# Kernel tuning notes

Measured on AMD Instinct MI355X. Metric: run time of the kernel, lower is better.

## Reference

```python
import jax, jax.numpy as jnp
import numpy as np
import math

B, S, D, H, FF, NB = 32, 512, 512, 8, 2048, 2
DK = D // H  # 64
NEG = -1e30  # stands in for torch's -1e32 (fp32-safe)


def _make_pe():
    # CosinePositionalEmbedding: deterministic sin/cos part (the 0.1*randn is fully overwritten)
    pos = np.arange(S, dtype=np.float32)[:, None]
    div = np.exp(np.arange(0, D, 2, dtype=np.float32) * -(math.log(10000.0) / D))
    pe = np.zeros((S, D), np.float32)
    pe[:, 0::2] = np.sin(pos * div)
    pe[:, 1::2] = np.cos(pos * div)
    return jnp.asarray(pe)[None]  # [1, S, D]


def setup_inputs() -> dict:
    key = jax.random.key(0)
    ks = jax.random.split(key, 10)
    def w(k, shape):
        return jax.random.normal(k, shape, jnp.float32) * 0.02
    return {
        "q_embed_data": jax.random.normal(ks[0], (B, S, D), jnp.float32),
        "qa_embed_data": jax.random.normal(ks[1], (B, S, D), jnp.float32),
        "forget_rate": jax.random.uniform(ks[2], (B, 1, S, 1), jnp.float32),
        "pe": _make_pe(),
        "Wk": w(ks[3], (NB, D, D)), "bk": jnp.zeros((NB, D), jnp.float32),
        "Wv": w(ks[4], (NB, D, D)), "bv": jnp.zeros((NB, D), jnp.float32),
        "Wo": w(ks[5], (NB, D, D)), "bo": jnp.zeros((NB, D), jnp.float32),
        "g1": jnp.ones((NB, D), jnp.float32), "be1": jnp.zeros((NB, D), jnp.float32),
        "W1": w(ks[6], (NB, D, FF)), "bf1": jnp.zeros((NB, FF), jnp.float32),
        "W2": w(ks[7], (NB, FF, D)), "bf2": jnp.zeros((NB, D), jnp.float32),
        "g2": jnp.ones((NB, D), jnp.float32), "be2": jnp.zeros((NB, D), jnp.float32),
    }


def _ln(x, g, b):
    m = jnp.mean(x, axis=-1, keepdims=True)
    v = jnp.var(x, axis=-1, keepdims=True)
    return (x - m) * jax.lax.rsqrt(v + 1e-5) * g + b


def reference(q_embed_data, qa_embed_data, forget_rate, pe, Wk, bk, Wv, bv, Wo, bo,
              g1, be1, W1, bf1, W2, bf2, g2, be2):
    x = q_embed_data + pe[:, :S]   # query stream
    y = qa_embed_data + pe[:, :S]  # value stream (constant across blocks)
    # mask==0 path: src_mask True where triu(k=0)==0, i.e. strictly-past positions j < i
    allowed = jnp.tril(jnp.ones((S, S), bool), k=-1)
    scale = 1.0 / math.sqrt(DK)
    for i in range(NB):
        # kq_same=True: q and k both use k_linear; query=key=x so q == k
        q = (x @ Wk[i] + bk[i]).reshape(B, S, H, DK).transpose(0, 2, 1, 3)  # [B,H,S,dk]
        k = q
        v = (y @ Wv[i] + bv[i]).reshape(B, S, H, DK).transpose(0, 2, 1, 3)
        scores = jnp.einsum('bhqd,bhkd->bhqk', q, k) * scale      # [B,H,S,S]
        scores = scores * forget_rate                              # broadcast [B,1,S,1]
        scores = jnp.where(allowed, scores, NEG)                   # masked_fill(mask==0, -1e32)
        attn = jax.nn.softmax(scores, axis=-1)
        attn = attn.at[:, :, 0, :].set(0.0)                        # zero_pad first query row
        out = jnp.einsum('bhqk,bhkd->bhqd', attn, v)
        out = out.transpose(0, 2, 1, 3).reshape(B, S, D) @ Wo[i] + bo[i]
        x = _ln(x + out, g1[i], be1[i])
        ffn = jax.nn.relu(x @ W1[i] + bf1[i]) @ W2[i] + bf2[i]
        x = _ln(x + ffn, g2[i], be2[i])
    return x
```

## Files before the change

### kernel.cpp

```cpp
#include <hip/hip_runtime.h>

#define B_ 32
#define S_ 512
#define D_ 512
#define H_ 8
#define DK_ 64
#define FF_ 2048

typedef float f32x4 __attribute__((ext_vector_type(4)));
typedef __bf16 bf16x8 __attribute__((ext_vector_type(8)));
typedef __bf16 bf16x4 __attribute__((ext_vector_type(4)));

__device__ __forceinline__ void gld_lds16(const void* gptr, void* lptr) {
    auto g = (__attribute__((address_space(1))) void*)(unsigned long long)gptr;
    auto l = (__attribute__((address_space(3))) void*)(unsigned)(unsigned long long)lptr;
    __builtin_amdgcn_global_load_lds(g, l, 16, 0, 0);
}

__global__ __launch_bounds__(256) void prep_kernel(
    const float* __restrict__ q, const float* __restrict__ qa,
    const float* __restrict__ pe, __bf16* __restrict__ xbf,
    __bf16* __restrict__ ybf)
{
    const int n4 = B_ * S_ * D_ / 4;
    for (int i = blockIdx.x * blockDim.x + threadIdx.x; i < n4;
         i += gridDim.x * blockDim.x) {
        float4 pv = ((const float4*)pe)[i & (S_ * D_ / 4 - 1)];
        float4 qv = ((const float4*)q)[i];
        float4 av = ((const float4*)qa)[i];
        bf16x4 xb = {(__bf16)(qv.x + pv.x), (__bf16)(qv.y + pv.y),
                     (__bf16)(qv.z + pv.z), (__bf16)(qv.w + pv.w)};
        ((bf16x4*)xbf)[i] = xb;
        bf16x4 yb = {(__bf16)(av.x + pv.x), (__bf16)(av.y + pv.y),
                     (__bf16)(av.z + pv.z), (__bf16)(av.w + pv.w)};
        ((bf16x4*)ybf)[i] = yb;
    }
}

__device__ __forceinline__ void ttile(
    const float* __restrict__ in, __bf16* __restrict__ out,
    int R, int C, int bx, int by, int t)
{
    __shared__ float tile[32][33];
    const int tc = bx * 32, tr = by * 32;
    const int lx = t & 31, ly = t >> 5;
    #pragma unroll
    for (int yy = ly; yy < 32; yy += 8)
        tile[yy][lx] = in[(long)(tr + yy) * C + tc + lx];
    __syncthreads();
    #pragma unroll
    for (int yy = ly; yy < 32; yy += 8)
        out[(long)(tc + yy) * R + tr + lx] = (__bf16)tile[lx][yy];
}

__global__ __launch_bounds__(256) void transpose_all(
    const float* __restrict__ Wk, const float* __restrict__ Wv,
    const float* __restrict__ Wo, const float* __restrict__ W1,
    const float* __restrict__ W2, __bf16* __restrict__ ok,
    __bf16* __restrict__ ov, __bf16* __restrict__ oo,
    __bf16* __restrict__ o1, __bf16* __restrict__ o2)
{
    const int id = blockIdx.x, t = threadIdx.x;
    if (id < 1536) {
        const int z = id >> 8, r = id & 255;
        const int sel = z >> 1, i = z & 1;
        const float* src = sel == 0 ? Wk : (sel == 1 ? Wv : Wo);
        __bf16* dst = sel == 0 ? ok : (sel == 1 ? ov : oo);
        ttile(src + (long)i * 262144, dst + (long)i * 262144, 512, 512,
              r & 15, r >> 4, t);
    } else if (id < 3584) {
        int r = id - 1536; const int i = r >> 10; r &= 1023;
        ttile(W1 + (long)i * 1048576, o1 + (long)i * 1048576, 512, 2048,
              r & 63, r >> 6, t);
    } else {
        int r = id - 3584; const int i = r >> 10; r &= 1023;
        ttile(W2 + (long)i * 1048576, o2 + (long)i * 1048576, 2048, 512,
              r & 15, r >> 4, t);
    }
}

template <int RELU, int MODE>
__global__ __launch_bounds__(256) void gemm_kernel(
    const __bf16* __restrict__ A, const __bf16* __restrict__ Bt,
    const float* __restrict__ bias, const __bf16* __restrict__ res,
    __bf16* __restrict__ out, int M, int N, int K)
{
    __shared__ __bf16 As[2][128 * 64];
    __shared__ __bf16 Bs[2][128 * 64];
    const int t = threadIdx.x;
    const int lane = t & 63;
    const int wv = t >> 6, wr = wv >> 1, wc = wv & 1;
    const int lr = lane & 15, lk = lane >> 4;

    const int nwg = gridDim.x * gridDim.y;
    const int lin = blockIdx.y * gridDim.x + blockIdx.x;
    const int swz = (lin & 7) * (nwg >> 3) + (lin >> 3);
    const int m0 = (swz / gridDim.x) * 128, n0 = (swz % gridDim.x) * 128;

    const int srow = t >> 3;
    const int sslot = (t & 7) ^ (srow & 7);
    const __bf16* gA = A + (long)(m0 + srow) * K + sslot * 8;
    const __bf16* gB = Bt + (long)(n0 + srow) * K + sslot * 8;
    const long rstep = (long)32 * K;

    auto STAGE = [&](int bsel, int k0) {
        char* ldsA = (char*)As[bsel] + t * 16;
        char* ldsB = (char*)Bs[bsel] + t * 16;
        #pragma unroll
        for (int u = 0; u < 4; ++u) {
            gld_lds16(gA + u * rstep + k0, ldsA + u * 4096);
            gld_lds16(gB + u * rstep + k0, ldsB + u * 4096);
        }
    };

    f32x4 acc[4][4] = {};
    auto COMPUTE = [&](int bsel) {
        #pragma unroll
        for (int kk = 0; kk < 2; ++kk) {
            bf16x8 af[4], bfr[4];
            #pragma unroll
            for (int i = 0; i < 4; ++i) {
                const int rr = wr * 64 + i * 16 + lr;
                af[i] = *(const bf16x8*)((const char*)As[bsel] +
                        (rr << 7) + (((kk * 4 + lk) ^ (rr & 7)) << 4));
            }
            #pragma unroll
            for (int j = 0; j < 4; ++j) {
                const int rr = wc * 64 + j * 16 + lr;
                bfr[j] = *(const bf16x8*)((const char*)Bs[bsel] +
                         (rr << 7) + (((kk * 4 + lk) ^ (rr & 7)) << 4));
            }
            #pragma unroll
            for (int i = 0; i < 4; ++i)
                #pragma unroll
                for (int j = 0; j < 4; ++j)
                    acc[i][j] = __builtin_amdgcn_mfma_f32_16x16x32_bf16(
                        af[i], bfr[j], acc[i][j], 0, 0, 0);
        }
    };

    const int NT = K >> 6;
    STAGE(0, 0);
    STAGE(1, 64);
    for (int kt = 0; kt < NT - 1; ++kt) {
        asm volatile("s_waitcnt vmcnt(8)" ::: "memory");
        __builtin_amdgcn_s_barrier();
        COMPUTE(kt & 1);
        __builtin_amdgcn_s_barrier();
        if (kt + 2 < NT) STAGE(kt & 1, (kt + 2) << 6);
    }
    asm volatile("s_waitcnt vmcnt(0)" ::: "memory");
    __builtin_amdgcn_s_barrier();
    COMPUTE((NT - 1) & 1);

    #pragma unroll
    for (int i = 0; i < 4; ++i) {
        #pragma unroll
        for (int j = 0; j < 4; ++j) {
            const int n = n0 + wc * 64 + j * 16 + lr;
            const float bv = bias[n];
            #pragma unroll
            for (int r = 0; r < 4; ++r) {
                const int m = m0 + wr * 64 + i * 16 + lk * 4 + r;
                const long off = (long)m * N + n;
                float v = acc[i][j][r] + bv;
                if (MODE == 1) v += (float)res[off];
                if (RELU) v = v > 0.f ? v : 0.f;
                out[off] = (__bf16)v;
            }
        }
    }
}

template <int RELU, int MODE>
__global__ __launch_bounds__(512, 2) void gemm8_kernel(
    const __bf16* __restrict__ A, const __bf16* __restrict__ Bt,
    const float* __restrict__ bias, const __bf16* __restrict__ res,
    __bf16* __restrict__ out, int M, int N, int K)
{
    __shared__ __bf16 lds[65536];
    const int t = threadIdx.x;
    const int lane = t & 63, wv = t >> 6;
    const int wr = wv >> 2, wc = wv & 3;
    const int lr = lane & 15, lk = lane >> 4;

    const int nwg = gridDim.x * gridDim.y;
    const int lin = blockIdx.y * gridDim.x + blockIdx.x;
    const int swz = (lin & 7) * (nwg >> 3) + (lin >> 3);
    const int m0 = (swz / gridDim.x) * 256, n0 = (swz % gridDim.x) * 256;

    const int srcrow = lane >> 2;
    const int srccol = ((lane & 3) ^ ((lane >> 4) & 3)) * 8;
    auto STG = [&](int isB, int kt2, int kk2, int pb) {
        const __bf16* src = isB ? Bt : A;
        const int base = isB ? n0 : m0;
        #pragma unroll
        for (int u = 0; u < 2; ++u) {
            const int sr = u * 8 + wv;
            const long g = (long)(base + sr * 16 + srcrow) * K + kt2 * 64 + kk2 * 32 + srccol;
            char* d = (char*)lds + pb * 65536 + isB * 32768 + ((sr * 2 + kk2) << 10) + lane * 16;
            gld_lds16(src + g, d);
        }
    };

    f32x4 acc[8][4] = {};
    bf16x8 af[4], bfr[4];
    auto RDA = [&](int p, int kk, int mh) {
        #pragma unroll
        for (int i = 0; i < 4; ++i) {
            const int sr = wr * 8 + mh * 4 + i;
            af[i] = *(const bf16x8*)((const char*)lds + p * 65536 +
                    ((sr * 2 + kk) << 10) + lr * 64 + ((lk ^ ((lr >> 2) & 3)) << 4));
        }
    };
    auto RDB = [&](int p, int kk) {
        #pragma unroll
        for (int j = 0; j < 4; ++j) {
            const int sr = wc * 4 + j;
            bfr[j] = *(const bf16x8*)((const char*)lds + p * 65536 + 32768 +
                     ((sr * 2 + kk) << 10) + lr * 64 + ((lk ^ ((lr >> 2) & 3)) << 4));
        }
    };
    auto MM = [&](int mh) {
        __builtin_amdgcn_s_setprio(1);
        #pragma unroll
        for (int i = 0; i < 4; ++i)
            #pragma unroll
            for (int j = 0; j < 4; ++j)
                acc[mh * 4 + i][j] = __builtin_amdgcn_mfma_f32_16x16x32_bf16(
                    af[i], bfr[j], acc[mh * 4 + i][j], 0, 0, 0);
        __builtin_amdgcn_s_setprio(0);
    };

    const int NT = K >> 6;
    STG(0, 0, 0, 0); STG(1, 0, 0, 0); STG(0, 0, 1, 0); STG(1, 0, 1, 0);
    STG(0, 1, 0, 1); STG(1, 1, 0, 1);

    for (int kt = 0; kt < NT - 1; ++kt) {
        const int p = kt & 1;
        asm volatile("s_waitcnt vmcnt(8)" ::: "memory");
        __builtin_amdgcn_s_barrier();
        RDA(p, 0, 0); RDB(p, 0); STG(0, kt + 1, 1, p ^ 1);
        MM(0);
        __builtin_amdgcn_s_barrier();
        RDA(p, 0, 1); STG(1, kt + 1, 1, p ^ 1);
        MM(1);
        asm volatile("s_waitcnt vmcnt(8)" ::: "memory");
        __builtin_amdgcn_s_barrier();
        RDA(p, 1, 0); RDB(p, 1); if (kt + 2 < NT) STG(0, kt + 2, 0, p);
        MM(0);
        __builtin_amdgcn_s_barrier();
        RDA(p, 1, 1); if (kt + 2 < NT) STG(1, kt + 2, 0, p);
        MM(1);
    }
    {
        const int p = (NT - 1) & 1;
        asm volatile("s_waitcnt vmcnt(4)" ::: "memory");
        __builtin_amdgcn_s_barrier();
        RDA(p, 0, 0); RDB(p, 0); MM(0);
        __builtin_amdgcn_s_barrier();
        RDA(p, 0, 1); MM(1);
        asm volatile("s_waitcnt vmcnt(0)" ::: "memory");
        __builtin_amdgcn_s_barrier();
        RDA(p, 1, 0); RDB(p, 1); MM(0);
        __builtin_amdgcn_s_barrier();
        RDA(p, 1, 1); MM(1);
    }

    #pragma unroll
    for (int i = 0; i < 8; ++i) {
        #pragma unroll
        for (int j = 0; j < 4; ++j) {
            const int n = n0 + wc * 64 + j * 16 + lr;
            const float bv = bias[n];
            #pragma unroll
            for (int r = 0; r < 4; ++r) {
                const int m = m0 + wr * 128 + i * 16 + lk * 4 + r;
                const long off = (long)m * N + n;
                float v = acc[i][j][r] + bv;
                if (MODE == 1) v += (float)res[off];
                if (RELU) v = v > 0.f ? v : 0.f;
                out[off] = (__bf16)v;
            }
        }
    }
}

__global__ __launch_bounds__(256) void gemm_kv(
    const __bf16* __restrict__ xbf, const __bf16* __restrict__ ybf,
    const __bf16* __restrict__ wkt, const __bf16* __restrict__ wvt,
    const float* __restrict__ bk, const float* __restrict__ bv,
    __bf16* __restrict__ kout, __bf16* __restrict__ vtout)
{
    constexpr int N = 512, K = 512;
    __shared__ __bf16 As[2][128 * 64];
    __shared__ __bf16 Bs[2][128 * 64];
    const int t = threadIdx.x;
    const int lane = t & 63;
    const int wv = t >> 6, wr = wv >> 1, wc = wv & 1;
    const int lr = lane & 15, lk = lane >> 4;
    const int zv = blockIdx.z;

    const __bf16* A  = zv ? ybf : xbf;
    const __bf16* Bt = zv ? wvt : wkt;
    const float* bias = zv ? bv : bk;
    __bf16* out = zv ? vtout : kout;

    const int nwg = gridDim.x * gridDim.y;
    const int lin = blockIdx.y * gridDim.x + blockIdx.x;
    const int swz = (lin & 7) * (nwg >> 3) + (lin >> 3);
    const int m0 = (swz / gridDim.x) * 128, n0 = (swz % gridDim.x) * 128;

    const int srow = t >> 3;
    const int sslot = (t & 7) ^ (srow & 7);
    const __bf16* gA = A + (long)(m0 + srow) * K + sslot * 8;
    const __bf16* gB = Bt + (long)(n0 + srow) * K + sslot * 8;
    const long rstep = (long)32 * K;

    auto STAGE = [&](int bsel, int k0) {
        char* ldsA = (char*)As[bsel] + t * 16;
        char* ldsB = (char*)Bs[bsel] + t * 16;
        #pragma unroll
        for (int u = 0; u < 4; ++u) {
            gld_lds16(gA + u * rstep + k0, ldsA + u * 4096);
            gld_lds16(gB + u * rstep + k0, ldsB + u * 4096);
        }
    };

    f32x4 acc[4][4] = {};
    auto COMPUTE = [&](int bsel) {
        #pragma unroll
        for (int kk = 0; kk < 2; ++kk) {
            bf16x8 af[4], bfr[4];
            #pragma unroll
            for (int i = 0; i < 4; ++i) {
                const int rr = wr * 64 + i * 16 + lr;
                af[i] = *(const bf16x8*)((const char*)As[bsel] +
                        (rr << 7) + (((kk * 4 + lk) ^ (rr & 7)) << 4));
            }
            #pragma unroll
            for (int j = 0; j < 4; ++j) {
                const int rr = wc * 64 + j * 16 + lr;
                bfr[j] = *(const bf16x8*)((const char*)Bs[bsel] +
                         (rr << 7) + (((kk * 4 + lk) ^ (rr & 7)) << 4));
            }
            #pragma unroll
            for (int i = 0; i < 4; ++i)
                #pragma unroll
                for (int j = 0; j < 4; ++j)
                    acc[i][j] = __builtin_amdgcn_mfma_f32_16x16x32_bf16(
                        af[i], bfr[j], acc[i][j], 0, 0, 0);
        }
    };

    const int NT = K >> 6;
    STAGE(0, 0);
    STAGE(1, 64);
    for (int kt = 0; kt < NT - 1; ++kt) {
        asm volatile("s_waitcnt vmcnt(8)" ::: "memory");
        __builtin_amdgcn_s_barrier();
        COMPUTE(kt & 1);
        __builtin_amdgcn_s_barrier();
        if (kt + 2 < NT) STAGE(kt & 1, (kt + 2) << 6);
    }
    asm volatile("s_waitcnt vmcnt(0)" ::: "memory");
    __builtin_amdgcn_s_barrier();
    COMPUTE((NT - 1) & 1);

    #pragma unroll
    for (int i = 0; i < 4; ++i) {
        #pragma unroll
        for (int j = 0; j < 4; ++j) {
            const int n = n0 + wc * 64 + j * 16 + lr;
            const float bvl = bias[n];
            if (zv) {
                const int mb = m0 + wr * 64 + i * 16 + lk * 4;
                const int b = mb >> 9, s = mb & 511;
                bf16x4 ov = {(__bf16)(acc[i][j][0] + bvl),
                             (__bf16)(acc[i][j][1] + bvl),
                             (__bf16)(acc[i][j][2] + bvl),
                             (__bf16)(acc[i][j][3] + bvl)};
                *(bf16x4*)(out + (((long)(b * 8 + (n >> 6)) * 64 + (n & 63)) << 9) + s) = ov;
            } else {
                #pragma unroll
                for (int r = 0; r < 4; ++r) {
                    const int m = m0 + wr * 64 + i * 16 + lk * 4 + r;
                    out[(long)m * N + n] = (__bf16)(acc[i][j][r] + bvl);
                }
            }
        }
    }
}

__global__ __launch_bounds__(256) void attn_kernel(
    const __bf16* __restrict__ Q, const __bf16* __restrict__ Vt,
    const float* __restrict__ fr, __bf16* __restrict__ Out)
{
    __shared__ __bf16 Ks[2][64 * 64];
    __shared__ __bf16 Vs[2][64 * 64];
    __shared__ __bf16 Plds[4][16 * 64];
    const int t = threadIdx.x;
    const int lane = t & 63, wv = t >> 6;
    const int lr = lane & 15, lk = lane >> 4;
    const int qb = blockIdx.x, h = blockIdx.y, b = blockIdx.z;
    const int qT = qb * 64 + wv * 16;

    const __bf16* qp = Q + (long)(b * S_ + qT + lr) * D_ + h * DK_ + lk * 8;
    const bf16x8 qf0 = *(const bf16x8*)qp;
    const bf16x8 qf1 = *(const bf16x8*)(qp + 32);

    float frv[4], ls[4];
    #pragma unroll
    for (int r = 0; r < 4; ++r) {
        frv[r] = fr[b * S_ + qT + lk * 4 + r] * 0.125f;
        ls[r] = 0.f;
    }
    f32x4 o[4] = {};

    const int srow = t >> 3;
    const int sslot = (t & 7) ^ (srow & 7);
    const __bf16* kstage = Q + (long)(b * S_ + srow) * D_ + h * DK_ + sslot * 8;
    const __bf16* vstage = Vt + ((long)(b * H_ + h) * DK_ + srow) * S_ + sslot * 8;
    __bf16* pl = &Plds[wv][0];
    const int sw = (lr & 7);

    auto STAGE = [&](int bsel, int ks) {
        gld_lds16(kstage + (long)ks * D_, (char*)Ks[bsel] + t * 16);
        gld_lds16(kstage + (long)(ks + 32) * D_, (char*)Ks[bsel] + 4096 + t * 16);
        gld_lds16(vstage + ks, (char*)Vs[bsel] + t * 16);
        gld_lds16(vstage + ks + 32 * S_, (char*)Vs[bsel] + 4096 + t * 16);
    };

    auto COMPUTE = [&](int bsel, int ks) {
        f32x4 sc[4] = {};
        #pragma unroll
        for (int j = 0; j < 4; ++j) {
            const char* kb = (const char*)Ks[bsel] + ((j * 16 + lr) << 7);
            const bf16x8 kf0 = *(const bf16x8*)(kb + ((lk ^ sw) << 4));
            const bf16x8 kf1 = *(const bf16x8*)(kb + (((lk + 4) ^ sw) << 4));
            sc[j] = __builtin_amdgcn_mfma_f32_16x16x32_bf16(qf0, kf0, sc[j], 0, 0, 0);
            sc[j] = __builtin_amdgcn_mfma_f32_16x16x32_bf16(qf1, kf1, sc[j], 0, 0, 0);
        }
        #pragma unroll
        for (int j = 0; j < 4; ++j) {
            const int col = ks + j * 16 + lr;
            const int c8 = j * 2 + (lr >> 3), cb = lr & 7;
            #pragma unroll
            for (int r = 0; r < 4; ++r) {
                const int row = lk * 4 + r;
                const int sidx = row * 64 + ((c8 ^ (row & 7)) << 3) + cb;
                const float e = __expf(sc[j][r] * frv[r]);
                const float p = (col < qT + row) ? e : 0.f;
                ls[r] += p;
                pl[sidx] = (__bf16)p;
            }
        }
        bf16x8 pf[2];
        #pragma unroll
        for (int kk = 0; kk < 2; ++kk) {
            const int ridx = lr * 64 + (((kk * 4 + lk) ^ sw) << 3);
            pf[kk] = *(const bf16x8*)&pl[ridx];
        }
        #pragma unroll
        for (int dt = 0; dt < 4; ++dt) {
            const char* vb = (const char*)Vs[bsel] + ((dt * 16 + lr) << 7);
            #pragma unroll
            for (int kk = 0; kk < 2; ++kk) {
                const bf16x8 vf = *(const bf16x8*)(vb + (((kk * 4 + lk) ^ sw) << 4));
                o[dt] = __builtin_amdgcn_mfma_f32_16x16x32_bf16(pf[kk], vf, o[dt], 0, 0, 0);
            }
        }
    };

    const int nt = qb + 1;
    STAGE(0, 0);
    if (nt > 1) STAGE(1, 64);
    for (int tt = 0; tt < nt - 1; ++tt) {
        asm volatile("s_waitcnt vmcnt(4)" ::: "memory");
        __builtin_amdgcn_s_barrier();
        COMPUTE(tt & 1, tt * 64);
        __builtin_amdgcn_s_barrier();
        if (tt + 2 < nt) STAGE(tt & 1, (tt + 2) * 64);
    }
    asm volatile("s_waitcnt vmcnt(0)" ::: "memory");
    __builtin_amdgcn_s_barrier();
    COMPUTE((nt - 1) & 1, (nt - 1) * 64);

    #pragma unroll
    for (int r = 0; r < 4; ++r) {
        #pragma unroll
        for (int d = 1; d < 16; d <<= 1)
            ls[r] += __shfl_xor(ls[r], d);
        const float inv = ls[r] > 0.f ? 1.f / ls[r] : 0.f;
        #pragma unroll
        for (int dt = 0; dt < 4; ++dt)
            Out[(long)(b * S_ + qT + lk * 4 + r) * D_ + h * DK_ + dt * 16 + lr] =
                (__bf16)(o[dt][r] * inv);
    }
}

__global__ __launch_bounds__(256) void ln_kernel(
    const __bf16* __restrict__ pre, const float* __restrict__ g,
    const float* __restrict__ be, float* __restrict__ xout,
    __bf16* __restrict__ xbf, int wf32)
{
    const int lane = threadIdx.x & 63, wv = threadIdx.x >> 6;
    const long row = (long)blockIdx.x * 4 + wv;
    const bf16x8 v = *(const bf16x8*)(pre + row * D_ + lane * 8);
    float f[8];
    #pragma unroll
    for (int k = 0; k < 8; ++k) f[k] = (float)v[k];
    float s = 0.f, ss = 0.f;
    #pragma unroll
    for (int k = 0; k < 8; ++k) { s += f[k]; ss += f[k] * f[k]; }
    #pragma unroll
    for (int d = 1; d < 64; d <<= 1) {
        s  += __shfl_xor(s, d);
        ss += __shfl_xor(ss, d);
    }
    const float mean = s * (1.f / 512.f);
    const float rstd = rsqrtf(ss * (1.f / 512.f) - mean * mean + 1e-5f);
    const float4 ga = ((const float4*)(g + lane * 8))[0];
    const float4 gc = ((const float4*)(g + lane * 8))[1];
    const float4 ba = ((const float4*)(be + lane * 8))[0];
    const float4 bc = ((const float4*)(be + lane * 8))[1];
    float o[8];
    o[0] = (f[0] - mean) * rstd * ga.x + ba.x;
    o[1] = (f[1] - mean) * rstd * ga.y + ba.y;
    o[2] = (f[2] - mean) * rstd * ga.z + ba.z;
    o[3] = (f[3] - mean) * rstd * ga.w + ba.w;
    o[4] = (f[4] - mean) * rstd * gc.x + bc.x;
    o[5] = (f[5] - mean) * rstd * gc.y + bc.y;
    o[6] = (f[6] - mean) * rstd * gc.z + bc.z;
    o[7] = (f[7] - mean) * rstd * gc.w + bc.w;
    bf16x8 xb = {(__bf16)o[0], (__bf16)o[1], (__bf16)o[2], (__bf16)o[3],
                 (__bf16)o[4], (__bf16)o[5], (__bf16)o[6], (__bf16)o[7]};
    *(bf16x8*)(xbf + row * D_ + lane * 8) = xb;
    if (wf32) {
        float* xo = xout + row * D_ + lane * 8;
        ((float4*)xo)[0] = make_float4(o[0], o[1], o[2], o[3]);
        ((float4*)xo)[1] = make_float4(o[4], o[5], o[6], o[7]);
    }
}

extern "C" void kernel_launch(void* const* d_in, const int* in_sizes, int n_in,
                              void* d_out, int out_size, void* d_ws, size_t ws_size,
                              hipStream_t stream) {
    const float* q_embed = (const float*)d_in[0];
    const float* qa_embed = (const float*)d_in[1];
    const float* fr  = (const float*)d_in[2];
    const float* pe  = (const float*)d_in[3];
    const float* Wk  = (const float*)d_in[4];
    const float* bk  = (const float*)d_in[5];
    const float* Wv  = (const float*)d_in[6];
    const float* bv  = (const float*)d_in[7];
    const float* Wo  = (const float*)d_in[8];
    const float* bo  = (const float*)d_in[9];
    const float* g1  = (const float*)d_in[10];
    const float* be1 = (const float*)d_in[11];
    const float* W1  = (const float*)d_in[12];
    const float* bf1 = (const float*)d_in[13];
    const float* W2  = (const float*)d_in[14];
    const float* bf2 = (const float*)d_in[15];
    const float* g2  = (const float*)d_in[16];
    const float* be2 = (const float*)d_in[17];

    char* ws = (char*)d_ws;
    __bf16* xbf   = (__bf16*)(ws + 0);
    __bf16* ybf   = (__bf16*)(ws + 16777216);
    __bf16* pool  = (__bf16*)(ws + 33554432);
    __bf16* preln = (__bf16*)(ws + 100663296);
    __bf16* wts   = (__bf16*)(ws + 117440512);

    __bf16* kbuf  = pool;
    __bf16* vtbuf = pool + 8388608;
    __bf16* abuf  = pool + 2 * 8388608;
    __bf16* f1buf = pool;

    __bf16* wkt = wts;
    __bf16* wvt = wts + 524288;
    __bf16* wot = wts + 1048576;
    __bf16* w1t = wts + 1572864;
    __bf16* w2t = wts + 3670016;

    transpose_all<<<5632, 256, 0, stream>>>(Wk, Wv, Wo, W1, W2,
                                            wkt, wvt, wot, w1t, w2t);
    prep_kernel<<<2048, 256, 0, stream>>>(q_embed, qa_embed, pe, xbf, ybf);

    for (int i = 0; i < 2; ++i) {
        gemm_kv<<<dim3(4, 128, 2), 256, 0, stream>>>(
            xbf, ybf, wkt + i * 262144, wvt + i * 262144,
            bk + i * 512, bv + i * 512, kbuf, vtbuf);
        attn_kernel<<<dim3(8, 8, 32), 256, 0, stream>>>(kbuf, vtbuf, fr, abuf);
        gemm_kernel<0, 1><<<dim3(4, 128), 256, 0, stream>>>(
            abuf, wot + i * 262144, bo + i * 512, xbf, preln, 16384, 512, 512);
        ln_kernel<<<4096, 256, 0, stream>>>(preln, g1 + i * 512, be1 + i * 512,
                                            (float*)d_out, xbf, 0);
        gemm8_kernel<1, 0><<<dim3(8, 64), 512, 0, stream>>>(
            xbf, w1t + i * 1048576, bf1 + i * 2048, nullptr, f1buf, 16384, 2048, 512);
        gemm_kernel<0, 1><<<dim3(4, 128), 256, 0, stream>>>(
            f1buf, w2t + i * 1048576, bf2 + i * 512, xbf, preln, 16384, 512, 2048);
        ln_kernel<<<4096, 256, 0, stream>>>(preln, g2 + i * 512, be2 + i * 512,
                                            (float*)d_out, xbf, i == 1 ? 1 : 0);
    }
}
```

Before: 432.2 us.

## Merge prep into weight-transpose launch, stage V-transpose epilogue via LDS, fold GEMM tail

Folds the input embedding/PE-add conversion into the weight-transpose kernel so both run in one launch. The gemm8 main loop absorbs its peeled final iteration, and its wait counts change to vmcnt(4) once per iteration with vmcnt(0) on the last. The K/V GEMM's transposed V output is now staged through swizzled shared memory and written as 16-byte row segments instead of scattered 8-byte stores. These target launch overhead and uncoalesced transposed writes, at the cost of an extra LDS round trip and two block barriers in the epilogue.

```diff
diff --git a/kernel.cpp b/kernel.cpp
--- a/kernel.cpp
+++ b/kernel.cpp
@@ -15,26 +15,6 @@
     auto g = (__attribute__((address_space(1))) void*)(unsigned long long)gptr;
     auto l = (__attribute__((address_space(3))) void*)(unsigned)(unsigned long long)lptr;
     __builtin_amdgcn_global_load_lds(g, l, 16, 0, 0);
-}
-
-__global__ __launch_bounds__(256) void prep_kernel(
-    const float* __restrict__ q, const float* __restrict__ qa,
-    const float* __restrict__ pe, __bf16* __restrict__ xbf,
-    __bf16* __restrict__ ybf)
-{
-    const int n4 = B_ * S_ * D_ / 4;
-    for (int i = blockIdx.x * blockDim.x + threadIdx.x; i < n4;
-         i += gridDim.x * blockDim.x) {
-        float4 pv = ((const float4*)pe)[i & (S_ * D_ / 4 - 1)];
-        float4 qv = ((const float4*)q)[i];
-        float4 av = ((const float4*)qa)[i];
-        bf16x4 xb = {(__bf16)(qv.x + pv.x), (__bf16)(qv.y + pv.y),
-                     (__bf16)(qv.z + pv.z), (__bf16)(qv.w + pv.w)};
-        ((bf16x4*)xbf)[i] = xb;
-        bf16x4 yb = {(__bf16)(av.x + pv.x), (__bf16)(av.y + pv.y),
-                     (__bf16)(av.z + pv.z), (__bf16)(av.w + pv.w)};
-        ((bf16x4*)ybf)[i] = yb;
-    }
 }
 
 __device__ __forceinline__ void ttile(
@@ -53,12 +33,15 @@
         out[(long)(tc + yy) * R + tr + lx] = (__bf16)tile[lx][yy];
 }
 
-__global__ __launch_bounds__(256) void transpose_all(
+__global__ __launch_bounds__(256) void pre_all(
     const float* __restrict__ Wk, const float* __restrict__ Wv,
     const float* __restrict__ Wo, const float* __restrict__ W1,
-    const float* __restrict__ W2, __bf16* __restrict__ ok,
-    __bf16* __restrict__ ov, __bf16* __restrict__ oo,
-    __bf16* __restrict__ o1, __bf16* __restrict__ o2)
+    const float* __restrict__ W2, const float* __restrict__ q,
+    const float* __restrict__ qa, const float* __restrict__ pe,
+    __bf16* __restrict__ ok, __bf16* __restrict__ ov,
+    __bf16* __restrict__ oo, __bf16* __restrict__ o1,
+    __bf16* __restrict__ o2, __bf16* __restrict__ xbf,
+    __bf16* __restrict__ ybf)
 {
     const int id = blockIdx.x, t = threadIdx.x;
     if (id < 1536) {
@@ -72,10 +55,23 @@
         int r = id - 1536; const int i = r >> 10; r &= 1023;
         ttile(W1 + (long)i * 1048576, o1 + (long)i * 1048576, 512, 2048,
               r & 63, r >> 6, t);
-    } else {
+    } else if (id < 5632) {
         int r = id - 3584; const int i = r >> 10; r &= 1023;
         ttile(W2 + (long)i * 1048576, o2 + (long)i * 1048576, 2048, 512,
               r & 15, r >> 4, t);
+    } else {
+        const int n4 = B_ * S_ * D_ / 4;
+        for (int i = (id - 5632) * 256 + t; i < n4; i += 2048 * 256) {
+            float4 pv = ((const float4*)pe)[i & (S_ * D_ / 4 - 1)];
+            float4 qv = ((const float4*)q)[i];
+            float4 av = ((const float4*)qa)[i];
+            bf16x4 xb = {(__bf16)(qv.x + pv.x), (__bf16)(qv.y + pv.y),
+                         (__bf16)(qv.z + pv.z), (__bf16)(qv.w + pv.w)};
+            ((bf16x4*)xbf)[i] = xb;
+            bf16x4 yb = {(__bf16)(av.x + pv.x), (__bf16)(av.y + pv.y),
+                         (__bf16)(av.z + pv.z), (__bf16)(av.w + pv.w)};
+            ((bf16x4*)ybf)[i] = yb;
+        }
     }
 }
 
@@ -236,35 +232,22 @@
     STG(0, 0, 0, 0); STG(1, 0, 0, 0); STG(0, 0, 1, 0); STG(1, 0, 1, 0);
     STG(0, 1, 0, 1); STG(1, 1, 0, 1);
 
-    for (int kt = 0; kt < NT - 1; ++kt) {
+    for (int kt = 0; kt < NT; ++kt) {
         const int p = kt & 1;
-        asm volatile("s_waitcnt vmcnt(8)" ::: "memory");
-        __builtin_amdgcn_s_barrier();
-        RDA(p, 0, 0); RDB(p, 0); STG(0, kt + 1, 1, p ^ 1);
+        if (kt == NT - 1) asm volatile("s_waitcnt vmcnt(0)" ::: "memory");
+        else              asm volatile("s_waitcnt vmcnt(4)" ::: "memory");
+        __builtin_amdgcn_s_barrier();
+        RDA(p, 0, 0); RDB(p, 0); if (kt + 1 < NT) STG(0, kt + 1, 1, p ^ 1);
         MM(0);
         __builtin_amdgcn_s_barrier();
-        RDA(p, 0, 1); STG(1, kt + 1, 1, p ^ 1);
+        RDA(p, 0, 1); if (kt + 1 < NT) STG(1, kt + 1, 1, p ^ 1);
         MM(1);
-        asm volatile("s_waitcnt vmcnt(8)" ::: "memory");
         __builtin_amdgcn_s_barrier();
         RDA(p, 1, 0); RDB(p, 1); if (kt + 2 < NT) STG(0, kt + 2, 0, p);
         MM(0);
         __builtin_amdgcn_s_barrier();
         RDA(p, 1, 1); if (kt + 2 < NT) STG(1, kt + 2, 0, p);
         MM(1);
-    }
-    {
-        const int p = (NT - 1) & 1;
-        asm volatile("s_waitcnt vmcnt(4)" ::: "memory");
-        __builtin_amdgcn_s_barrier();
-        RDA(p, 0, 0); RDB(p, 0); MM(0);
-        __builtin_amdgcn_s_barrier();
-        RDA(p, 0, 1); MM(1);
-        asm volatile("s_waitcnt vmcnt(0)" ::: "memory");
-        __builtin_amdgcn_s_barrier();
-        RDA(p, 1, 0); RDB(p, 1); MM(0);
-        __builtin_amdgcn_s_barrier();
-        RDA(p, 1, 1); MM(1);
     }
 
     #pragma unroll
@@ -367,21 +350,48 @@
     __builtin_amdgcn_s_barrier();
     COMPUTE((NT - 1) & 1);
 
-    #pragma unroll
-    for (int i = 0; i < 4; ++i) {
-        #pragma unroll
-        for (int j = 0; j < 4; ++j) {
-            const int n = n0 + wc * 64 + j * 16 + lr;
-            const float bvl = bias[n];
-            if (zv) {
-                const int mb = m0 + wr * 64 + i * 16 + lk * 4;
-                const int b = mb >> 9, s = mb & 511;
-                bf16x4 ov = {(__bf16)(acc[i][j][0] + bvl),
-                             (__bf16)(acc[i][j][1] + bvl),
-                             (__bf16)(acc[i][j][2] + bvl),
-                             (__bf16)(acc[i][j][3] + bvl)};
-                *(bf16x4*)(out + (((long)(b * 8 + (n >> 6)) * 64 + (n & 63)) << 9) + s) = ov;
-            } else {
+    if (zv) {
+        __syncthreads();
+        __bf16* st = (__bf16*)As;
+        #pragma unroll
+        for (int i = 0; i < 4; ++i) {
+            #pragma unroll
+            for (int j = 0; j < 4; ++j) {
+                const int nl = wc * 64 + j * 16 + lr;
+                const float bvl = bias[n0 + nl];
+                #pragma unroll
+                for (int r = 0; r < 4; ++r) {
+                    const int ml = wr * 64 + i * 16 + lk * 4 + r;
+                    const int m16 = ml >> 3;
+                    st[nl * 128 + (((m16 ^ (nl & 15)) << 3) | (ml & 7))] =
+                        (__bf16)(acc[i][j][r] + bvl);
+                }
+            }
+        }
+        __syncthreads();
+        const int rowh = t >> 2, c4 = t & 3;
+        const int b = m0 >> 9;
+        #pragma unroll
+        for (int pass = 0; pass < 2; ++pass) {
+            const int row = pass * 64 + rowh;
+            const int n = n0 + row;
+            __bf16* dst = out + (((long)((b * 8 + (n >> 6)) * 64 + (n & 63))) << 9)
+                          + (m0 & 511);
+            #pragma unroll
+            for (int seg = 0; seg < 4; ++seg) {
+                const int m16 = seg * 4 + c4;
+                const bf16x8 vv =
+                    *(const bf16x8*)&st[row * 128 + ((m16 ^ (row & 15)) << 3)];
+                *(bf16x8*)(dst + m16 * 8) = vv;
+            }
+        }
+    } else {
+        #pragma unroll
+        for (int i = 0; i < 4; ++i) {
+            #pragma unroll
+            for (int j = 0; j < 4; ++j) {
+                const int n = n0 + wc * 64 + j * 16 + lr;
+                const float bvl = bias[n];
                 #pragma unroll
                 for (int r = 0; r < 4; ++r) {
                     const int m = m0 + wr * 64 + i * 16 + lk * 4 + r;
@@ -583,9 +593,8 @@
     __bf16* w1t = wts + 1572864;
     __bf16* w2t = wts + 3670016;
 
-    transpose_all<<<5632, 256, 0, stream>>>(Wk, Wv, Wo, W1, W2,
-                                            wkt, wvt, wot, w1t, w2t);
-    prep_kernel<<<2048, 256, 0, stream>>>(q_embed, qa_embed, pe, xbf, ybf);
+    pre_all<<<7680, 256, 0, stream>>>(Wk, Wv, Wo, W1, W2, q_embed, qa_embed, pe,
+                                      wkt, wvt, wot, w1t, w2t, xbf, ybf);
 
     for (int i = 0; i < 2; ++i) {
         gemm_kv<<<dim3(4, 128, 2), 256, 0, stream>>>(
```

After: 428.8 us. No clear change (-0.8%).
